# Optimization experiments

Hardware: AMD Instinct MI355X
Metric: run time of the kernel (lower is better)

Reference implementation:

```python
import jax, jax.numpy as jnp
import numpy as np

DIM = 1024
HEADS = 16
DHEAD = 64
WIDTH = 512
INNER = HEADS * DHEAD  # 1024
BATCH = 2
SEQ = 4096  # divisible by WIDTH -> 8 blocks


def setup_inputs() -> dict:
    key = jax.random.key(0)
    ks = jax.random.split(key, 6)
    x = jax.random.normal(ks[0], (BATCH, SEQ, DIM), jnp.float32)
    # bias broadcast over (b, w) onto sim of shape [b, w, h, WIDTH, 2*WIDTH]
    rel_pos_bias = jax.random.normal(ks[1], (HEADS, WIDTH, 2 * WIDTH), jnp.float32)
    # stacked (past_k, past_v), each [b, h, WIDTH, d]
    xl_memories = jax.random.normal(ks[2], (2, BATCH, HEADS, WIDTH, DHEAD), jnp.float32)
    gamma = jnp.ones((DIM,), jnp.float32)
    w_qkv = jax.random.normal(ks[3], (DIM, 3 * INNER), jnp.float32) * 0.02
    w_out = jax.random.normal(ks[4], (INNER, DIM), jnp.float32) * 0.02
    return {"x": x, "rel_pos_bias": rel_pos_bias, "xl_memories": xl_memories,
            "gamma": gamma, "w_qkv": w_qkv, "w_out": w_out}


def reference(x, rel_pos_bias, xl_memories, gamma, w_qkv, w_out):
    b, seq, dim = x.shape
    w = seq // WIDTH
    # LayerNorm (beta buffer is zeros in the module)
    mu = jnp.mean(x, axis=-1, keepdims=True)
    var = jnp.var(x, axis=-1, keepdims=True)
    xn = (x - mu) * jax.lax.rsqrt(var + 1e-5) * gamma
    # qkv projection, split heads, blockify: [b, w, h, WIDTH, d]
    qkv = xn @ w_qkv
    q, k, v = jnp.split(qkv, 3, axis=-1)
    def to_blocks(t):
        return t.reshape(b, w, WIDTH, HEADS, DHEAD).transpose(0, 1, 3, 2, 4)
    bq, bk, bv = map(to_blocks, (q, k, v))
    # new XL memories: last block's k/v -> [2, b, h, WIDTH, d]
    memories = jnp.stack((bk[:, -1], bv[:, -1]))
    # prepend past block of k/v
    past_k = xl_memories[0][:, None]  # [b, 1, h, WIDTH, d]
    past_v = xl_memories[1][:, None]
    bk = jnp.concatenate((past_k, bk), axis=1)  # [b, w+1, h, WIDTH, d]
    bv = jnp.concatenate((past_v, bv), axis=1)
    # sliding 2-block kv window: [b, w, h, 2*WIDTH, d]
    bk = jnp.concatenate((bk[:, :-1], bk[:, 1:]), axis=-2)
    bv = jnp.concatenate((bv[:, :-1], bv[:, 1:]), axis=-2)
    # attention with rel-pos bias and causal mask (i=WIDTH queries, j=2*WIDTH keys)
    scale = DHEAD ** -0.5
    sim = jnp.einsum('bwhid,bwhjd->bwhij', bq, bk) * scale + rel_pos_bias
    i, j = WIDTH, 2 * WIDTH
    causal_mask = jnp.triu(jnp.ones((i, j), bool), j - i + 1)
    neg = -jnp.finfo(sim.dtype).max
    sim = jnp.where(causal_mask, neg, sim)
    attn = jax.nn.softmax(sim, axis=-1)
    out = jnp.einsum('bwhij,bwhjd->bwhid', attn, bv)
    # merge blocks and heads back: [b, seq, inner]
    out = out.transpose(0, 1, 3, 2, 4).reshape(b, seq, INNER)
    out = out[:, :seq]
    return out @ w_out, memories
```

## Files before the change

kernel.cpp:

```cpp
#include <hip/hip_runtime.h>
#include <hip/hip_bf16.h>

#define DIMV   1024
#define HEADSV 16
#define DHEADV 64
#define WIDTHV 512
#define INNERV 1024
#define BATCHV 2
#define SEQV   4096
#define NROWS  (BATCHV*SEQV)
#define KVROWS (WIDTHV + SEQV)

#define LOG2E 1.4426950408889634f

typedef short bf16x8 __attribute__((ext_vector_type(8)));
typedef short bf16x4 __attribute__((ext_vector_type(4)));
typedef int   int4v  __attribute__((ext_vector_type(4)));
typedef float f32x4  __attribute__((ext_vector_type(4)));

typedef const __attribute__((address_space(1))) void* gvp;
typedef __attribute__((address_space(3))) void* lvp;

static __device__ __forceinline__ short f2bf(float f) {
  __hip_bfloat16 h = __float2bfloat16(f);
  return __builtin_bit_cast(short, h);
}
static __device__ __forceinline__ float bf2f(short s) {
  unsigned u = ((unsigned)(unsigned short)s) << 16;
  return __builtin_bit_cast(float, u);
}
static __device__ __forceinline__ bf16x8 ntload8(const short* p) {
  int4v v = __builtin_nontemporal_load((const int4v*)p);
  return __builtin_bit_cast(bf16x8, v);
}

__global__ __launch_bounds__(256) void ln_kernel(const float* __restrict__ x,
                                                 const float* __restrict__ gamma,
                                                 short* __restrict__ xn) {
  int row = blockIdx.x;
  int t = threadIdx.x;
  const float* xr = x + (size_t)row * DIMV;
  float4 v = reinterpret_cast<const float4*>(xr)[t];
  float s  = v.x + v.y + v.z + v.w;
  float sq = v.x*v.x + v.y*v.y + v.z*v.z + v.w*v.w;
  #pragma unroll
  for (int o = 32; o > 0; o >>= 1) { s += __shfl_down(s, o); sq += __shfl_down(sq, o); }
  __shared__ float red[8];
  int wv = t >> 6;
  if ((t & 63) == 0) { red[wv] = s; red[4 + wv] = sq; }
  __syncthreads();
  s  = red[0] + red[1] + red[2] + red[3];
  sq = red[4] + red[5] + red[6] + red[7];
  float mean = s * (1.0f/1024.0f);
  float var  = sq * (1.0f/1024.0f) - mean*mean;
  float rstd = rsqrtf(var + 1e-5f);
  float4 g = reinterpret_cast<const float4*>(gamma)[t];
  short4 o4;
  o4.x = f2bf((v.x - mean) * rstd * g.x);
  o4.y = f2bf((v.y - mean) * rstd * g.y);
  o4.z = f2bf((v.z - mean) * rstd * g.z);
  o4.w = f2bf((v.w - mean) * rstd * g.w);
  reinterpret_cast<short4*>(xn + (size_t)row * DIMV)[t] = o4;
}

__global__ __launch_bounds__(256) void transpose_f32_bf16(const float* __restrict__ in,
                                                          short* __restrict__ out,
                                                          int R, int C) {
  __shared__ float tile[32][33];
  int tc = blockIdx.x * 32;
  int tr = blockIdx.y * 32;
  int tx = threadIdx.x & 31, ty = threadIdx.x >> 5;
  #pragma unroll
  for (int i = 0; i < 32; i += 8)
    tile[ty + i][tx] = in[(size_t)(tr + ty + i) * C + tc + tx];
  __syncthreads();
  #pragma unroll
  for (int i = 0; i < 32; i += 8)
    out[(size_t)(tc + ty + i) * R + tr + tx] = f2bf(tile[tx][ty + i]);
}

__global__ __launch_bounds__(256) void pack_bias(const float* __restrict__ in,
                                                 short* __restrict__ out) {
  int idx = blockIdx.x * 256 + threadIdx.x;
  int j   = idx & 1023;
  int ir4 = (idx >> 10) & 127;
  int h   = idx >> 17;
  const float* src = in + ((size_t)(h*512 + ir4*4))*1024 + j;
  short4 o;
  o.x = f2bf(src[0]    * LOG2E);
  o.y = f2bf(src[1024] * LOG2E);
  o.z = f2bf(src[2048] * LOG2E);
  o.w = f2bf(src[3072] * LOG2E);
  *reinterpret_cast<short4*>(out + (size_t)idx*4) = o;
}

__global__ void xl_to_kv(const float* __restrict__ xl,
                         short* __restrict__ k_all, short* __restrict__ v_all) {
  int tid = blockIdx.x * 256 + threadIdx.x;
  int d = (tid & 15) * 4;
  int rest = tid >> 4;
  int s = rest & 511; rest >>= 9;
  int h = rest & 15;  rest >>= 4;
  int b = rest & 1;   int m2 = rest >> 1;
  float4 v = *reinterpret_cast<const float4*>(
      xl + ((((size_t)((m2*2 + b)*16 + h))*512 + s)*64 + d));
  short4 o; o.x = f2bf(v.x); o.y = f2bf(v.y); o.z = f2bf(v.z); o.w = f2bf(v.w);
  short* dst = (m2 ? v_all : k_all) + (((size_t)(b*16 + h)*KVROWS + s)*64 + d);
  *reinterpret_cast<short4*>(dst) = o;
}

__global__ __launch_bounds__(256) void transpose_v(const short* __restrict__ v,
                                                   short* __restrict__ vt) {
  __shared__ __align__(16) short tile[64][72];
  int bh = blockIdx.y;
  int s0 = blockIdx.x * 64;
  int tid = threadIdx.x;
  const short* src = v + (size_t)bh * KVROWS * 64;
  #pragma unroll
  for (int p = 0; p < 2; ++p) {
    int flat = p*256 + tid;
    int row = flat >> 3, ch = flat & 7;
    int pch = ch ^ (row >> 3);
    *reinterpret_cast<int4v*>(&tile[row][pch*8]) =
      *reinterpret_cast<const int4v*>(src + (size_t)(s0 + row)*64 + ch*8);
  }
  __syncthreads();
  short* dst = vt + (size_t)bh * 64 * KVROWS;
  #pragma unroll
  for (int p = 0; p < 2; ++p) {
    int flat = p*256 + tid;
    int d = flat >> 3, sch = flat & 7;
    short tmp[8];
    #pragma unroll
    for (int k = 0; k < 8; ++k) {
      int s = sch*8 + k;
      int pch = (d >> 3) ^ (s >> 3);
      tmp[k] = tile[s][pch*8 + (d & 7)];
    }
    *reinterpret_cast<int4v*>(dst + (size_t)d*KVROWS + s0 + sch*8) =
      *reinterpret_cast<const int4v*>(tmp);
  }
}

template<int MODE>
__global__ __launch_bounds__(256) void gemm_bt(
    const short* __restrict__ A, const short* __restrict__ Bm,
    short* __restrict__ qo, short* __restrict__ ko, short* __restrict__ vo,
    float* __restrict__ memo, float* __restrict__ co, int N) {
  __shared__ __align__(16) short As[128*32];
  __shared__ __align__(16) short Bs[128*32];
  const int K = 1024;
  int bm = blockIdx.x * 128;
  int bn = blockIdx.y * 128;
  int tid = threadIdx.x;
  int lane = tid & 63, wid = tid >> 6;
  int wr = wid >> 1, wc = wid & 1;
  int fr = lane & 15, fq = lane >> 4;

  f32x4 acc[4][4] = {};

  for (int k0 = 0; k0 < K; k0 += 32) {
    #pragma unroll
    for (int p = 0; p < 2; ++p) {
      int flat = p*256 + wid*64 + lane;
      int row = flat >> 2;
      int ch  = (lane & 3) ^ (row & 3);
      __builtin_amdgcn_global_load_lds(
          (gvp)(const void*)(A + (size_t)(bm + row)*K + k0 + ch*8),
          (lvp)(void*)(As + (size_t)(p*256 + wid*64)*8), 16, 0, 0);
      __builtin_amdgcn_global_load_lds(
          (gvp)(const void*)(Bm + (size_t)(bn + row)*K + k0 + ch*8),
          (lvp)(void*)(Bs + (size_t)(p*256 + wid*64)*8), 16, 0, 0);
    }
    __syncthreads();
    bf16x8 af[4], bfr[4];
    #pragma unroll
    for (int i = 0; i < 4; ++i) {
      int ra = wr*64 + i*16 + fr;
      int rb = wc*64 + i*16 + fr;
      af[i]  = *reinterpret_cast<const bf16x8*>(&As[ra*32 + (fq ^ (ra & 3))*8]);
      bfr[i] = *reinterpret_cast<const bf16x8*>(&Bs[rb*32 + (fq ^ (rb & 3))*8]);
    }
    #pragma unroll
    for (int i = 0; i < 4; ++i)
      #pragma unroll
      for (int j = 0; j < 4; ++j)
        acc[i][j] = __builtin_amdgcn_mfma_f32_16x16x32_bf16(af[i], bfr[j], acc[i][j], 0, 0, 0);
    __syncthreads();
  }

  if (MODE == 0) {
    #pragma unroll
    for (int i = 0; i < 4; ++i)
      #pragma unroll
      for (int j = 0; j < 4; ++j)
        #pragma unroll
        for (int r = 0; r < 4; ++r) {
          int m = bm + wr*64 + i*16 + fq*4 + r;
          int n = bn + wc*64 + j*16 + fr;
          float val = acc[i][j][r];
          int b = m >> 12, s = m & 4095;
          if (n < 1024) {
            qo[(size_t)m*1024 + n] = f2bf(val * (0.125f * LOG2E));
          } else {
            int h = (n >> 6) & 15, d = n & 63;
            size_t idx = ((size_t)((b << 4) + h)*KVROWS + 512 + s)*64 + d;
            if (n < 2048) ko[idx] = f2bf(val);
            else          vo[idx] = f2bf(val);
            if (s >= 3584) {
              int m2 = (n < 2048) ? 0 : 1;
              memo[((size_t)(((m2*2 + b) << 4) + h)*512 + (s - 3584))*64 + d] = val;
            }
          }
        }
  } else {
    #pragma unroll
    for (int i = 0; i < 4; ++i)
      #pragma unroll
      for (int j = 0; j < 4; ++j)
        #pragma unroll
        for (int r = 0; r < 4; ++r) {
          int m = bm + wr*64 + i*16 + fq*4 + r;
          int n = bn + wc*64 + j*16 + fr;
          co[(size_t)m*N + n] = acc[i][j][r];
        }
  }
}

__global__ __launch_bounds__(256, 2) void attn_kernel(
    const short* __restrict__ q,
    const short* __restrict__ k_all,
    const short* __restrict__ vt,
    const short* __restrict__ bp,
    short* __restrict__ attnb) {
  __shared__ __align__(16) short Ks[2][64*72];
  __shared__ __align__(16) short Vs[2][64*72];
  __shared__ __align__(16) short Pb[4][16*72];

  const int bid = blockIdx.x;
  const int h = bid & 15, w = (bid >> 4) & 7, b = (bid >> 7) & 1, cq = bid >> 8;
  const int tid = threadIdx.x, lane = tid & 63, wid = tid >> 6;
  const int fr = lane & 15, fq = lane >> 4;
  const int qoff = cq*128 + wid*32;

  const short* qrow = q + ((size_t)(b*SEQV + w*WIDTHV + qoff))*1024 + h*64;
  bf16x8 qf[2][2];
  #pragma unroll
  for (int i = 0; i < 2; ++i)
    #pragma unroll
    for (int c = 0; c < 2; ++c)
      qf[i][c] = ntload8(qrow + (size_t)(i*16 + fr)*1024 + c*32 + fq*8);

  f32x4 o[2][4] = {};
  float racc[2][4] = {{0.f,0.f,0.f,0.f},{0.f,0.f,0.f,0.f}};

  const short* kg  = k_all + ((size_t)(b*16 + h)*KVROWS + w*512)*64;
  const short* vg  = vt    + (size_t)(b*16 + h)*64*KVROWS + w*512;
  const short* bpw = bp    + ((size_t)(h*128 + (qoff >> 2) + fq))*4096;

  const int sr = tid >> 3, sc = tid & 7;
  const short* kgs = kg + (size_t)sr*64 + sc*8;
  const short* vgs = vg + (size_t)sr*KVROWS + sc*8;
  const int soA = sr*72 + sc*8;

  {
    int4v k0v[2], v0v[2];
    #pragma unroll
    for (int p = 0; p < 2; ++p) {
      k0v[p] = *reinterpret_cast<const int4v*>(kgs + p*32*64);
      v0v[p] = *reinterpret_cast<const int4v*>(vgs + (size_t)p*32*KVROWS);
    }
    #pragma unroll
    for (int p = 0; p < 2; ++p) {
      *reinterpret_cast<int4v*>(&Ks[0][soA + p*2304]) = k0v[p];
      *reinterpret_cast<int4v*>(&Vs[0][soA + p*2304]) = v0v[p];
    }
  }
  __syncthreads();

  const int NT = 2*cq + 10;
  const int tmaxw = 2*cq + 8 + (wid >> 1);

  for (int t = 0; t < NT; ++t) {
    const int buf = t & 1;
    int4v kk[2], vv[2];
    const bool more = (t + 1 < NT);
    if (more) {
      #pragma unroll
      for (int p = 0; p < 2; ++p) {
        kk[p] = *reinterpret_cast<const int4v*>(kgs + (size_t)(t+1)*4096 + p*32*64);
        vv[p] = *reinterpret_cast<const int4v*>(vgs + (t+1)*64 + (size_t)p*32*KVROWS);
      }
    }
    if (t <= tmaxw) {
      const int j0 = t * 64;
      bf16x4 bb[2][4];
      #pragma unroll
      for (int i = 0; i < 2; ++i)
        #pragma unroll
        for (int jc = 0; jc < 4; ++jc)
          bb[i][jc] = *reinterpret_cast<const bf16x4*>(
              &bpw[(size_t)i*16384 + (size_t)(j0 + jc*16 + fr)*4]);
      bf16x8 kf0[4], kf1[4];
      #pragma unroll
      for (int jc = 0; jc < 4; ++jc) {
        kf0[jc] = *reinterpret_cast<const bf16x8*>(&Ks[buf][(jc*16 + fr)*72 + fq*8]);
        kf1[jc] = *reinterpret_cast<const bf16x8*>(&Ks[buf][(jc*16 + fr)*72 + 32 + fq*8]);
      }
      bf16x8 vf[2][4];
      #pragma unroll
      for (int jk = 0; jk < 2; ++jk)
        #pragma unroll
        for (int dc = 0; dc < 4; ++dc)
          vf[jk][dc] = *reinterpret_cast<const bf16x8*>(
              &Vs[buf][(dc*16 + fr)*72 + jk*32 + fq*8]);

      f32x4 s[2][4];
      __builtin_amdgcn_s_setprio(1);
      #pragma unroll
      for (int i = 0; i < 2; ++i)
        #pragma unroll
        for (int jc = 0; jc < 4; ++jc) {
          f32x4 c;
          c[0] = bf2f(bb[i][jc][0]); c[1] = bf2f(bb[i][jc][1]);
          c[2] = bf2f(bb[i][jc][2]); c[3] = bf2f(bb[i][jc][3]);
          s[i][jc] = __builtin_amdgcn_mfma_f32_16x16x32_bf16(qf[i][0], kf0[jc], c, 0, 0, 0);
        }
      #pragma unroll
      for (int i = 0; i < 2; ++i)
        #pragma unroll
        for (int jc = 0; jc < 4; ++jc)
          s[i][jc] = __builtin_amdgcn_mfma_f32_16x16x32_bf16(qf[i][1], kf1[jc], s[i][jc], 0, 0, 0);
      __builtin_amdgcn_s_setprio(0);

      if (t == tmaxw) {
        #pragma unroll
        for (int i = 0; i < 2; ++i)
          #pragma unroll
          for (int jc = 0; jc < 4; ++jc)
            #pragma unroll
            for (int r = 0; r < 4; ++r)
              if (j0 + jc*16 + fr > qoff + i*16 + fq*4 + r + 512)
                s[i][jc][r] = -1e30f;
      }

      #pragma unroll
      for (int i = 0; i < 2; ++i) {
        short* Pw = &Pb[wid][0];
        #pragma unroll
        for (int jc = 0; jc < 4; ++jc)
          #pragma unroll
          for (int r = 0; r < 4; ++r) {
            float p = exp2f(fminf(s[i][jc][r], 80.f));
            racc[i][r] += p;
            Pw[(fq*4 + r)*72 + jc*16 + fr] = f2bf(p);
          }
        asm volatile("s_waitcnt lgkmcnt(0)" ::: "memory");
        __builtin_amdgcn_sched_barrier(0);
        __builtin_amdgcn_s_setprio(1);
        #pragma unroll
        for (int jk = 0; jk < 2; ++jk) {
          bf16x8 pf = *reinterpret_cast<const bf16x8*>(&Pw[fr*72 + jk*32 + fq*8]);
          #pragma unroll
          for (int dc = 0; dc < 4; ++dc)
            o[i][dc] = __builtin_amdgcn_mfma_f32_16x16x32_bf16(pf, vf[jk][dc], o[i][dc], 0, 0, 0);
        }
        __builtin_amdgcn_s_setprio(0);
        __builtin_amdgcn_sched_barrier(0);
      }
    }
    if (more) {
      #pragma unroll
      for (int p = 0; p < 2; ++p) {
        *reinterpret_cast<int4v*>(&Ks[buf ^ 1][soA + p*2304]) = kk[p];
        *reinterpret_cast<int4v*>(&Vs[buf ^ 1][soA + p*2304]) = vv[p];
      }
    }
    __syncthreads();
  }

  #pragma unroll
  for (int i = 0; i < 2; ++i)
    #pragma unroll
    for (int off = 1; off < 16; off <<= 1)
      #pragma unroll
      for (int r = 0; r < 4; ++r)
        racc[i][r] += __shfl_xor(racc[i][r], off);

  short* obase = attnb + ((size_t)(b*SEQV + w*WIDTHV + qoff))*1024 + h*64;
  #pragma unroll
  for (int i = 0; i < 2; ++i) {
    float inv[4];
    #pragma unroll
    for (int r = 0; r < 4; ++r) inv[r] = 1.0f / racc[i][r];
    #pragma unroll
    for (int dc = 0; dc < 4; ++dc)
      #pragma unroll
      for (int r = 0; r < 4; ++r)
        obase[(size_t)(i*16 + fq*4 + r)*1024 + dc*16 + fr] = f2bf(o[i][dc][r] * inv[r]);
  }
}

extern "C" void kernel_launch(void* const* d_in, const int* in_sizes, int n_in,
                              void* d_out, int out_size, void* d_ws, size_t ws_size,
                              hipStream_t stream) {
  const float* x     = (const float*)d_in[0];
  const float* bias  = (const float*)d_in[1];
  const float* xl    = (const float*)d_in[2];
  const float* gamma = (const float*)d_in[3];
  const float* w_qkv = (const float*)d_in[4];
  const float* w_out = (const float*)d_in[5];
  float* out = (float*)d_out;
  float* mem_out = out + (size_t)BATCHV*SEQV*DIMV;

  char* ws = (char*)d_ws;
  size_t off = 0;
  auto alloc = [&](size_t bytes) { size_t o = off; off += (bytes + 255) & ~(size_t)255; return o; };
  short* xn    = (short*)(ws + alloc((size_t)NROWS*DIMV*2));
  short* wqkvT = (short*)(ws + alloc((size_t)3*INNERV*DIMV*2));
  short* woutT = (short*)(ws + alloc((size_t)DIMV*INNERV*2));
  short* bp    = (short*)(ws + alloc((size_t)HEADSV*128*1024*4*2));
  short* qbuf  = (short*)(ws + alloc((size_t)NROWS*INNERV*2));
  short* k_all = (short*)(ws + alloc((size_t)BATCHV*HEADSV*KVROWS*DHEADV*2));
  short* v_all = (short*)(ws + alloc((size_t)BATCHV*HEADSV*KVROWS*DHEADV*2));
  short* vt    = (short*)(ws + alloc((size_t)BATCHV*HEADSV*KVROWS*DHEADV*2));
  short* attnb = xn;

  transpose_f32_bf16<<<dim3(3*INNERV/32, DIMV/32), 256, 0, stream>>>(w_qkv, wqkvT, DIMV, 3*INNERV);
  transpose_f32_bf16<<<dim3(INNERV/32, DIMV/32), 256, 0, stream>>>(w_out, woutT, DIMV, INNERV);
  pack_bias<<<8192, 256, 0, stream>>>(bias, bp);
  xl_to_kv<<<2048, 256, 0, stream>>>(xl, k_all, v_all);
  ln_kernel<<<NROWS, 256, 0, stream>>>(x, gamma, xn);
  gemm_bt<0><<<dim3(NROWS/128, (3*INNERV)/128), 256, 0, stream>>>(
      xn, wqkvT, qbuf, k_all, v_all, mem_out, nullptr, 3*INNERV);
  transpose_v<<<dim3(KVROWS/64, BATCHV*HEADSV), 256, 0, stream>>>(v_all, vt);
  attn_kernel<<<4*BATCHV*8*HEADSV, 256, 0, stream>>>(qbuf, k_all, vt, bp, attnb);
  gemm_bt<1><<<dim3(NROWS/128, INNERV/128), 256, 0, stream>>>(
      attnb, woutT, nullptr, nullptr, nullptr, nullptr, out, INNERV);
}
```

Baseline: 233.1 us.

## Double-buffer GEMM LDS tiles with BK=64 to overlap global loads with MFMA

The bf16 GEMM kernel now uses two LDS buffers with a K-tile of 64 instead of one buffer with a K-tile of 32. Each iteration issues async global-to-LDS loads for the next tile before running MFMAs on the current one, and the swizzle widens to 8 chunks. This halves the number of barriers per K loop and hides global load latency behind compute. In exchange, LDS use per block rises to 64KB, which may reduce occupancy.

Measured after the change: 206.0 us. 1.13x faster.

```diff
diff --git a/kernel.cpp b/kernel.cpp
--- a/kernel.cpp
+++ b/kernel.cpp
@@ -147,8 +147,8 @@
     const short* __restrict__ A, const short* __restrict__ Bm,
     short* __restrict__ qo, short* __restrict__ ko, short* __restrict__ vo,
     float* __restrict__ memo, float* __restrict__ co, int N) {
-  __shared__ __align__(16) short As[128*32];
-  __shared__ __align__(16) short Bs[128*32];
+  __shared__ __align__(16) short As[2][128*64];
+  __shared__ __align__(16) short Bs[2][128*64];
   const int K = 1024;
   int bm = blockIdx.x * 128;
   int bn = blockIdx.y * 128;
@@ -157,35 +157,51 @@
   int wr = wid >> 1, wc = wid & 1;
   int fr = lane & 15, fq = lane >> 4;
 
+  const int r0 = tid >> 3;
+  const int sl = tid & 7;
+  const int sc = sl ^ (r0 & 7);
+  const short* agp = A  + (size_t)(bm + r0)*K + sc*8;
+  const short* bgp = Bm + (size_t)(bn + r0)*K + sc*8;
+  const int wbase = wid*64*8;
+
   f32x4 acc[4][4] = {};
 
-  for (int k0 = 0; k0 < K; k0 += 32) {
-    #pragma unroll
-    for (int p = 0; p < 2; ++p) {
-      int flat = p*256 + wid*64 + lane;
-      int row = flat >> 2;
-      int ch  = (lane & 3) ^ (row & 3);
+  auto stage = [&](int bufi, int k0) {
+    #pragma unroll
+    for (int p = 0; p < 4; ++p) {
       __builtin_amdgcn_global_load_lds(
-          (gvp)(const void*)(A + (size_t)(bm + row)*K + k0 + ch*8),
-          (lvp)(void*)(As + (size_t)(p*256 + wid*64)*8), 16, 0, 0);
+          (gvp)(const void*)(agp + (size_t)p*32*K + k0),
+          (lvp)(void*)(&As[bufi][p*2048 + wbase]), 16, 0, 0);
       __builtin_amdgcn_global_load_lds(
-          (gvp)(const void*)(Bm + (size_t)(bn + row)*K + k0 + ch*8),
-          (lvp)(void*)(Bs + (size_t)(p*256 + wid*64)*8), 16, 0, 0);
-    }
-    __syncthreads();
-    bf16x8 af[4], bfr[4];
-    #pragma unroll
-    for (int i = 0; i < 4; ++i) {
-      int ra = wr*64 + i*16 + fr;
-      int rb = wc*64 + i*16 + fr;
-      af[i]  = *reinterpret_cast<const bf16x8*>(&As[ra*32 + (fq ^ (ra & 3))*8]);
-      bfr[i] = *reinterpret_cast<const bf16x8*>(&Bs[rb*32 + (fq ^ (rb & 3))*8]);
-    }
-    #pragma unroll
-    for (int i = 0; i < 4; ++i)
-      #pragma unroll
-      for (int j = 0; j < 4; ++j)
-        acc[i][j] = __builtin_amdgcn_mfma_f32_16x16x32_bf16(af[i], bfr[j], acc[i][j], 0, 0, 0);
+          (gvp)(const void*)(bgp + (size_t)p*32*K + k0),
+          (lvp)(void*)(&Bs[bufi][p*2048 + wbase]), 16, 0, 0);
+    }
+  };
+
+  stage(0, 0);
+  __syncthreads();
+
+  for (int it = 0; it < 16; ++it) {
+    const int buf = it & 1;
+    if (it < 15) stage(buf ^ 1, (it + 1) * 64);
+    __builtin_amdgcn_sched_barrier(0);
+    #pragma unroll
+    for (int kc = 0; kc < 2; ++kc) {
+      const int ca = kc*4 + fq;
+      bf16x8 af[4], bfr[4];
+      #pragma unroll
+      for (int i = 0; i < 4; ++i) {
+        int ra = wr*64 + i*16 + fr;
+        int rb = wc*64 + i*16 + fr;
+        af[i]  = *reinterpret_cast<const bf16x8*>(&As[buf][ra*64 + (ca ^ (ra & 7))*8]);
+        bfr[i] = *reinterpret_cast<const bf16x8*>(&Bs[buf][rb*64 + (ca ^ (rb & 7))*8]);
+      }
+      #pragma unroll
+      for (int i = 0; i < 4; ++i)
+        #pragma unroll
+        for (int j = 0; j < 4; ++j)
+          acc[i][j] = __builtin_amdgcn_mfma_f32_16x16x32_bf16(af[i], bfr[j], acc[i][j], 0, 0, 0);
+    }
     __syncthreads();
   }
 
```
